# Performance work log

Hardware: AMD Instinct MI355X
Metric: run time of the kernel (lower is better)

## Reference

```python
import math
import jax, jax.numpy as jnp
import numpy as np

B, QC, KC, RES, SRC = 4, 512, 256, 64, 128
T = RES * RES


def setup_inputs():
    key = jax.random.key(0)
    ks = jax.random.split(key, 8)
    return {
        "key_feat": jax.random.normal(ks[0], (B, KC, SRC, SRC), jnp.float32),
        "query": jax.random.normal(ks[1], (B, QC, RES, RES), jnp.float32),
        "Weight_Mat": jax.random.uniform(ks[2], (B, T, T), dtype=jnp.float32),
        "key_proj_w": jax.random.normal(ks[3], (QC, KC), jnp.float32) * 0.02,
        "norm_w": jnp.ones((QC,), jnp.float32),
        "norm_b": jnp.zeros((QC,), jnp.float32),
        "qkv_w": jax.random.normal(ks[4], (3 * QC, 2 * QC), jnp.float32) * 0.02,
        "qkv_b": jax.random.normal(ks[5], (3 * QC,), jnp.float32) * 0.02,
        "proj_w": jax.random.normal(ks[6], (QC, QC), jnp.float32) * 0.02,
        "proj_b": jnp.zeros((QC,), jnp.float32),
    }


def group_norm(x, w, b, groups=32, eps=1e-5):
    # x: (b, C, L) -- GroupNorm over channel groups and spatial dim
    bs, C, L = x.shape
    xg = x.reshape(bs, groups, C // groups, L)
    mu = xg.mean(axis=(2, 3), keepdims=True)
    var = xg.var(axis=(2, 3), keepdims=True)
    xn = ((xg - mu) * jax.lax.rsqrt(var + eps)).reshape(bs, C, L)
    return xn * w[None, :, None] + b[None, :, None]


def reference(key_feat, query, Weight_Mat, key_proj_w, norm_w, norm_b, qkv_w, qkv_b, proj_w, proj_b):
    b, qc, H, W = query.shape
    f = key_feat.shape[2] // H  # exact integer downsample factor (2)
    # F.interpolate bilinear (align_corners=False) at exact 1/f rate == f x f average pooling
    kds = key_feat.reshape(b, key_feat.shape[1], H, f, W, f).mean(axis=(3, 5))
    # Weight_Mat interpolate has scale==1 in source (no-op), elided.
    k = jnp.einsum('oc,bchw->bohw', key_proj_w, kds).reshape(b, qc, H * W)
    q = query.reshape(b, qc, H * W)
    q = group_norm(q, norm_w, norm_b)
    k = group_norm(k, norm_w, norm_b)
    # qkv: 1x1 conv1d on concat(q, k) -> (b, 3*qc, T)
    qkv = jnp.einsum('oc,bct->bot', qkv_w, jnp.concatenate([q, k], axis=1)) + qkv_b[None, :, None]
    qq, kk, vv = jnp.split(qkv, 3, axis=1)  # each (b, qc, T); num_heads=1 so ch=qc
    scale = qc ** -0.25  # 1/sqrt(sqrt(ch))
    logits = Weight_Mat * jnp.einsum('bct,bcs->bts', qq * scale, kk * scale)
    attn = jax.nn.softmax(logits, axis=-1)
    a = jnp.einsum('bts,bcs->bct', attn, vv)
    h = jnp.einsum('oc,bct->bot', proj_w, a) + proj_b[None, :, None]
    # residual uses the NORMALIZED query, as in the source
    return (q + h).reshape(b, qc, H, W)
```

## Files before the change

### kernel.cpp

```cpp
#include <hip/hip_runtime.h>
#include <hip/hip_bf16.h>
#include <stdint.h>

#define NB 4
#define CQ 512
#define CK 256
#define TT 4096
#define SCALE_QK 0.21022410381342863f

using bf16x8 = __attribute__((ext_vector_type(8))) short;
using f32x4  = __attribute__((ext_vector_type(4))) float;
using u32x4  = __attribute__((ext_vector_type(4))) unsigned int;
typedef unsigned short u16;

__device__ __forceinline__ u16 f2bf(float f) {
    union { float f; unsigned u; } v; v.f = f;
    return (u16)((v.u + 0x7fffu + ((v.u >> 16) & 1u)) >> 16);
}
__device__ __forceinline__ float bf2f(u16 h) {
    union { float f; unsigned u; } v; v.u = ((unsigned)h) << 16;
    return v.f;
}
__device__ __forceinline__ bf16x8 pack8(f32x4 a, f32x4 b) {
    bf16x8 r;
    r[0] = (short)f2bf(a[0]); r[1] = (short)f2bf(a[1]);
    r[2] = (short)f2bf(a[2]); r[3] = (short)f2bf(a[3]);
    r[4] = (short)f2bf(b[0]); r[5] = (short)f2bf(b[1]);
    r[6] = (short)f2bf(b[2]); r[7] = (short)f2bf(b[3]);
    return r;
}
__device__ __forceinline__ void gload_lds16(const void* g, void* l) {
    __builtin_amdgcn_global_load_lds(
        (const __attribute__((address_space(1))) unsigned int*)g,
        (__attribute__((address_space(3))) unsigned int*)l, 16, 0, 0);
}

__global__ __launch_bounds__(256) void wconv_kernel(const float* __restrict__ src,
        u16* __restrict__ dst, int n, int scale_until) {
    int i = (blockIdx.x * 256 + threadIdx.x) * 8;
    if (i >= n) return;
    f32x4 a = *(const f32x4*)(src + i);
    f32x4 c = *(const f32x4*)(src + i + 4);
    if (i < scale_until) {
        a *= SCALE_QK;
        c *= SCALE_QK;
    }
    *(bf16x8*)(dst + i) = pack8(a, c);
}

__global__ __launch_bounds__(256) void pool_tr_kernel(const float* __restrict__ kf,
                                                      u16* __restrict__ kdsT) {
    int h = blockIdx.x, b = blockIdx.y;
    __shared__ u16 tile[64][264];
    for (int idx = threadIdx.x; idx < 64 * 256; idx += 256) {
        int w = idx & 63, c = idx >> 6;
        const float* base = kf + (((size_t)b * CK + c) * 128 + 2 * h) * 128 + 2 * w;
        float2 r0 = *(const float2*)base;
        float2 r1 = *(const float2*)(base + 128);
        tile[w][c] = f2bf(0.25f * (r0.x + r0.y + r1.x + r1.y));
    }
    __syncthreads();
    for (int idx = threadIdx.x; idx < 64 * 32; idx += 256) {
        int w = idx >> 5, cg = (idx & 31) << 3;
        *(u32x4*)(kdsT + ((size_t)b * TT + h * 64 + w) * CK + cg) = *(const u32x4*)&tile[w][cg];
    }
}

template <int ISBF>
__global__ __launch_bounds__(256) void gn_stats_kernel(const void* __restrict__ xv,
        const float* __restrict__ gw, const float* __restrict__ gb,
        float* __restrict__ sc, float* __restrict__ sh) {
    int g = blockIdx.x, b = blockIdx.y;
    size_t base = ((size_t)b * CQ + g * 16) * TT;
    float s = 0.f, q = 0.f;
    for (int i = threadIdx.x * 4; i < 16 * TT; i += 256 * 4) {
        float v0, v1, v2, v3;
        if constexpr (ISBF) {
            const u16* x = (const u16*)xv;
            uint2 u = *(const uint2*)(x + base + i);
            v0 = bf2f((u16)(u.x & 0xffff)); v1 = bf2f((u16)(u.x >> 16));
            v2 = bf2f((u16)(u.y & 0xffff)); v3 = bf2f((u16)(u.y >> 16));
        } else {
            const float* x = (const float*)xv;
            f32x4 v = *(const f32x4*)(x + base + i);
            v0 = v[0]; v1 = v[1]; v2 = v[2]; v3 = v[3];
        }
        s += v0 + v1 + v2 + v3;
        q += v0 * v0 + v1 * v1 + v2 * v2 + v3 * v3;
    }
#pragma unroll
    for (int d = 1; d < 64; d <<= 1) { s += __shfl_xor(s, d, 64); q += __shfl_xor(q, d, 64); }
    __shared__ float shs[4], shq[4];
    int wid = threadIdx.x >> 6;
    if ((threadIdx.x & 63) == 0) { shs[wid] = s; shq[wid] = q; }
    __syncthreads();
    if (threadIdx.x < 16) {
        float S = shs[0] + shs[1] + shs[2] + shs[3];
        float Q = shq[0] + shq[1] + shq[2] + shq[3];
        const float inv = 1.f / (16.f * TT);
        float mean = S * inv, var = Q * inv - mean * mean;
        float rstd = rsqrtf(var + 1e-5f);
        int c = g * 16 + threadIdx.x;
        float w = gw[c] * rstd;
        sc[b * CQ + c] = w;
        sh[b * CQ + c] = gb[c] - mean * w;
    }
}

template <int ISBF>
__global__ __launch_bounds__(256) void affine_tr_kernel(const void* __restrict__ xv,
        const float* __restrict__ sc, const float* __restrict__ sh, u16* __restrict__ out) {
    int t0 = blockIdx.x * 64, c0 = blockIdx.y * 64, b = blockIdx.z;
    __shared__ u16 tile[64][72];
    for (int idx = threadIdx.x; idx < 64 * 64; idx += 256) {
        int tl = idx & 63, cl = idx >> 6;
        int c = c0 + cl;
        float v;
        if constexpr (ISBF) v = bf2f(((const u16*)xv)[((size_t)b * CQ + c) * TT + t0 + tl]);
        else                v = ((const float*)xv)[((size_t)b * CQ + c) * TT + t0 + tl];
        tile[tl][cl] = f2bf(v * sc[b * CQ + c] + sh[b * CQ + c]);
    }
    __syncthreads();
    for (int idx = threadIdx.x; idx < 64 * 8; idx += 256) {
        int tl = idx >> 3, cg = (idx & 7) << 3;
        *(u32x4*)(out + ((size_t)b * TT + t0 + tl) * CQ + c0 + cg) = *(const u32x4*)&tile[tl][cg];
    }
}

template <int EPI, int CONCAT, int SWAP>
__global__ __launch_bounds__(256) void gemm_st_kernel(
        const u16* __restrict__ Wb, const u16* __restrict__ X1, const u16* __restrict__ X2,
        int Ktot, const float* __restrict__ bias,
        u16* __restrict__ outb, u16* __restrict__ outb2, float* __restrict__ outf,
        const float* __restrict__ query, const float* __restrict__ qsc,
        const float* __restrict__ qsh) {
    int b = blockIdx.z;
    int o0 = blockIdx.x * 128, t0 = blockIdx.y * 128;
    int wid = threadIdx.x >> 6, lane = threadIdx.x & 63;
    int lr = lane & 15, lg = lane >> 4;
    int osub = (wid >> 1) * 64, tsub = (wid & 1) * 64;

    __shared__ u16 Wl[2][128][64];
    __shared__ u16 Xl[2][128][64];

    const int Kx = CONCAT ? 512 : Ktot;
    int srow = lane >> 3;
    int sxw = ((lane & 7) ^ srow) << 4;
    int xr = (lr & 7) << 4;

    f32x4 acc[4][4];
#pragma unroll
    for (int i = 0; i < 4; i++)
#pragma unroll
        for (int j = 0; j < 4; j++) acc[i][j] = f32x4{0.f, 0.f, 0.f, 0.f};

    int nk = Ktot >> 6;

#define STAGE_TILE(KC, BUF)                                                          \
    do {                                                                             \
        int c0_ = (KC) << 6;                                                         \
        const u16* xs_;                                                              \
        if (CONCAT && c0_ >= 512) xs_ = X2 + ((size_t)b * TT) * 512 + (c0_ - 512);   \
        else if (CONCAT)          xs_ = X1 + ((size_t)b * TT) * 512 + c0_;           \
        else                      xs_ = X1 + ((size_t)b * TT) * (size_t)Ktot + c0_;  \
        const char* xb_ = (const char*)(xs_ + (size_t)(t0 + wid * 32) * Kx) + sxw;   \
        const char* wb_ = (const char*)(Wb + (size_t)(o0 + wid * 32) * Ktot + c0_) + sxw; \
        _Pragma("unroll")                                                            \
        for (int i_ = 0; i_ < 4; i_++) {                                             \
            gload_lds16(xb_ + (size_t)(i_ * 8 + srow) * (Kx * 2),                    \
                        &Xl[BUF][wid * 32 + i_ * 8][0]);                             \
            gload_lds16(wb_ + (size_t)(i_ * 8 + srow) * (Ktot * 2),                  \
                        &Wl[BUF][wid * 32 + i_ * 8][0]);                             \
        }                                                                            \
    } while (0)

    STAGE_TILE(0, 0);
    __syncthreads();
    int cur = 0;
    for (int kc = 0; kc < nk; kc++) {
        if (kc + 1 < nk) STAGE_TILE(kc + 1, cur ^ 1);
#pragma unroll
        for (int kk = 0; kk < 2; kk++) {
            int boff = (kk * 64 + lg * 16) ^ xr;
            bf16x8 am[4], bn[4];
#pragma unroll
            for (int mi = 0; mi < 4; mi++) {
                if (SWAP) am[mi] = *(const bf16x8*)((const char*)&Xl[cur][tsub + mi * 16 + lr][0] + boff);
                else      am[mi] = *(const bf16x8*)((const char*)&Wl[cur][osub + mi * 16 + lr][0] + boff);
            }
#pragma unroll
            for (int ni = 0; ni < 4; ni++) {
                if (SWAP) bn[ni] = *(const bf16x8*)((const char*)&Wl[cur][osub + ni * 16 + lr][0] + boff);
                else      bn[ni] = *(const bf16x8*)((const char*)&Xl[cur][tsub + ni * 16 + lr][0] + boff);
            }
#pragma unroll
            for (int mi = 0; mi < 4; mi++)
#pragma unroll
                for (int ni = 0; ni < 4; ni++)
                    acc[mi][ni] = __builtin_amdgcn_mfma_f32_16x16x32_bf16(am[mi], bn[ni], acc[mi][ni], 0, 0, 0);
        }
        __syncthreads();
        cur ^= 1;
    }
#undef STAGE_TILE

    if (SWAP) {
#pragma unroll
        for (int mi = 0; mi < 4; mi++)
#pragma unroll
            for (int ni = 0; ni < 4; ni++)
#pragma unroll
                for (int reg = 0; reg < 4; reg++) {
                    int t = t0 + tsub + mi * 16 + 4 * lg + reg;
                    int o = o0 + osub + ni * 16 + lr;
                    float v = acc[mi][ni][reg] + bias[o] * SCALE_QK;
                    if (o < 512) outb[((size_t)b * TT + t) * 512 + o] = f2bf(v);
                    else         outb2[((size_t)b * TT + t) * 512 + (o - 512)] = f2bf(v);
                }
    } else {
#pragma unroll
        for (int mi = 0; mi < 4; mi++)
#pragma unroll
            for (int reg = 0; reg < 4; reg++) {
                int o = o0 + osub + mi * 16 + 4 * lg + reg;
                float bv = (EPI >= 1) ? bias[o] : 0.f;
#pragma unroll
                for (int ni = 0; ni < 4; ni++) {
                    int t = t0 + tsub + ni * 16 + lr;
                    size_t oidx = ((size_t)b * CQ + o) * TT + t;
                    float v = acc[mi][ni][reg] + bv;
                    if (EPI == 2) {
                        outf[oidx] = v + query[oidx] * qsc[b * CQ + o] + qsh[b * CQ + o];
                    } else {
                        outb[oidx] = f2bf(v);
                    }
                }
            }
    }
}

__global__ __launch_bounds__(512, 2) void flash_kernel(
        const u16* __restrict__ qqT, const u16* __restrict__ kkT,
        const u16* __restrict__ vv, const float* __restrict__ WM,
        u16* __restrict__ aT) {
    int b = blockIdx.y;
    int T0 = blockIdx.x * 64;
    int wid = threadIdx.x >> 6, lane = threadIdx.x & 63;
    int lr = lane & 15, lg = lane >> 4;
    int tb = wid >> 1, sb = wid & 1;

    __shared__ u16 K_lds[64][512];
    __shared__ u16 V_lds[512][64];
    __shared__ u16 p_lds[64][64];
    __shared__ float ex_max[64][2];
    __shared__ float ex_sum[64][2];

    bf16x8 qf[16];
    {
        const u16* qrow = qqT + ((size_t)b * TT + T0 + 16 * tb + lr) * CQ + lg * 8;
#pragma unroll
        for (int kc = 0; kc < 16; kc++) qf[kc] = *(const bf16x8*)(qrow + kc * 32);
    }
    f32x4 acc[16];
#pragma unroll
    for (int i = 0; i < 16; i++) acc[i] = f32x4{0.f, 0.f, 0.f, 0.f};
    float m[4], l[4];
#pragma unroll
    for (int r = 0; r < 4; r++) { m[r] = -1e30f; l[r] = 0.f; }

    const float* wmrow = WM + ((size_t)b * TT + T0 + 16 * tb + 4 * lg) * TT + 32 * sb + lr;
    const char* kbase = (const char*)(kkT + ((size_t)b * TT) * CQ);
    int myt = 16 * tb + 4 * lg;

    for (int s0 = 0; s0 < TT; s0 += 64) {
        __syncthreads();
#pragma unroll
        for (int i = 0; i < 8; i++) {
            int s = wid * 8 + i;
            gload_lds16(kbase + ((size_t)(s0 + s)) * 1024 + ((lane ^ (s & 7)) << 4),
                        &K_lds[s][0]);
        }
#pragma unroll
        for (int g2 = 0; g2 < 8; g2++) {
            int c0 = (wid * 8 + g2) * 8;
            int c = c0 + (lane >> 3);
            gload_lds16((const char*)(vv + ((size_t)b * CQ + c) * TT + s0) +
                            ((((lane & 7) ^ (c & 7))) << 4),
                        &V_lds[c0][0]);
        }
        float wmv[2][4];
#pragma unroll
        for (int fs = 0; fs < 2; fs++)
#pragma unroll
            for (int reg = 0; reg < 4; reg++)
                wmv[fs][reg] = wmrow[(size_t)reg * TT + s0 + fs * 16];
        __syncthreads();

        f32x4 sacc[2];
        sacc[0] = f32x4{0.f, 0.f, 0.f, 0.f};
        sacc[1] = f32x4{0.f, 0.f, 0.f, 0.f};
#pragma unroll
        for (int kc = 0; kc < 16; kc++) {
#pragma unroll
            for (int fs = 0; fs < 2; fs++) {
                const char* kp = (const char*)&K_lds[32 * sb + fs * 16 + lr][0];
                bf16x8 kfr = *(const bf16x8*)(kp + ((((kc << 2) | lg) ^ (lr & 7)) << 4));
                sacc[fs] = __builtin_amdgcn_mfma_f32_16x16x32_bf16(qf[kc], kfr, sacc[fs], 0, 0, 0);
            }
        }
        float lgt[2][4], pmax[4];
#pragma unroll
        for (int r = 0; r < 4; r++) pmax[r] = -3e38f;
#pragma unroll
        for (int fs = 0; fs < 2; fs++)
#pragma unroll
            for (int reg = 0; reg < 4; reg++) {
                float v = sacc[fs][reg] * wmv[fs][reg];
                lgt[fs][reg] = v;
                pmax[reg] = fmaxf(pmax[reg], v);
            }
#pragma unroll
        for (int d = 1; d < 16; d <<= 1)
#pragma unroll
            for (int reg = 0; reg < 4; reg++)
                pmax[reg] = fmaxf(pmax[reg], __shfl_xor(pmax[reg], d, 64));
        if (lr == 0) {
#pragma unroll
            for (int reg = 0; reg < 4; reg++) ex_max[myt + reg][sb] = pmax[reg];
        }
        __syncthreads();
        float fac[4], rsum[4];
#pragma unroll
        for (int reg = 0; reg < 4; reg++) {
            int t = myt + reg;
            float mn = fmaxf(m[reg], fmaxf(ex_max[t][0], ex_max[t][1]));
            fac[reg] = __expf(m[reg] - mn);
            m[reg] = mn;
            rsum[reg] = 0.f;
        }
#pragma unroll
        for (int fs = 0; fs < 2; fs++)
#pragma unroll
            for (int reg = 0; reg < 4; reg++) {
                float p = __expf(lgt[fs][reg] - m[reg]);
                rsum[reg] += p;
                int t = myt + reg;
                int s = 32 * sb + fs * 16 + lr;
                *(u16*)((char*)p_lds + t * 128 + ((((s >> 3) ^ (t & 7))) << 4) + ((s & 7) << 1)) = f2bf(p);
            }
#pragma unroll
        for (int d = 1; d < 16; d <<= 1)
#pragma unroll
            for (int reg = 0; reg < 4; reg++)
                rsum[reg] += __shfl_xor(rsum[reg], d, 64);
        if (lr == 0) {
#pragma unroll
            for (int reg = 0; reg < 4; reg++) ex_sum[myt + reg][sb] = rsum[reg];
        }
        __syncthreads();
#pragma unroll
        for (int reg = 0; reg < 4; reg++) {
            int t = myt + reg;
            l[reg] = l[reg] * fac[reg] + ex_sum[t][0] + ex_sum[t][1];
        }
#pragma unroll
        for (int nt = 0; nt < 16; nt++)
#pragma unroll
            for (int reg = 0; reg < 4; reg++) acc[nt][reg] *= fac[reg];
#pragma unroll
        for (int ks = 0; ks < 2; ks++) {
            int prow = 16 * tb + lr;
            bf16x8 pa = *(const bf16x8*)((const char*)p_lds + prow * 128 +
                                         ((((ks << 2) | lg) ^ (lr & 7)) << 4));
#pragma unroll
            for (int nt = 0; nt < 16; nt++) {
                int vr = 256 * sb + nt * 16 + lr;
                bf16x8 vf = *(const bf16x8*)((const char*)&V_lds[vr][0] +
                                             ((((ks << 2) | lg) ^ (lr & 7)) << 4));
                acc[nt] = __builtin_amdgcn_mfma_f32_16x16x32_bf16(pa, vf, acc[nt], 0, 0, 0);
            }
        }
    }
    float inv[4];
#pragma unroll
    for (int reg = 0; reg < 4; reg++) inv[reg] = 1.f / l[reg];
#pragma unroll
    for (int nt = 0; nt < 16; nt++)
#pragma unroll
        for (int reg = 0; reg < 4; reg++) {
            int t = T0 + myt + reg;
            int c = 256 * sb + nt * 16 + lr;
            aT[((size_t)b * TT + t) * CQ + c] = f2bf(acc[nt][reg] * inv[reg]);
        }
}

extern "C" void kernel_launch(void* const* d_in, const int* in_sizes, int n_in,
                              void* d_out, int out_size, void* d_ws, size_t ws_size,
                              hipStream_t stream) {
    const float* key_feat = (const float*)d_in[0];
    const float* query    = (const float*)d_in[1];
    const float* WM       = (const float*)d_in[2];
    const float* kpw      = (const float*)d_in[3];
    const float* norm_w   = (const float*)d_in[4];
    const float* norm_b   = (const float*)d_in[5];
    const float* qkv_w    = (const float*)d_in[6];
    const float* qkv_b    = (const float*)d_in[7];
    const float* proj_w   = (const float*)d_in[8];
    const float* proj_b   = (const float*)d_in[9];
    float* out = (float*)d_out;
    char* ws = (char*)d_ws;

    u16* kdsT = (u16*)(ws);
    u16* kraw = (u16*)(ws + 8388608);
    u16* qnT  = (u16*)(ws + 25165824);
    u16* knT  = (u16*)(ws + 41943040);
    u16* qqT  = (u16*)(ws + 58720256);
    u16* kkT  = (u16*)(ws + 75497472);
    u16* vvp  = (u16*)(ws + 92274688);
    u16* aT   = (u16*)(ws);
    u16* wqkv = (u16*)(ws + 16777216);
    u16* wproj= (u16*)(ws + 19922944);
    float* qsc = (float*)(ws + 109051904);
    float* qsh = qsc + NB * CQ;
    float* ksc = qsh + NB * CQ;
    float* ksh = ksc + NB * CQ;
    u16* wkp  = (u16*)(ws + 109084672);

    wconv_kernel<<<64, 256, 0, stream>>>(kpw, wkp, 512 * 256, 0);
    pool_tr_kernel<<<dim3(64, NB), 256, 0, stream>>>(key_feat, kdsT);
    gemm_st_kernel<0, 0, 0><<<dim3(4, 32, NB), 256, 0, stream>>>(
        wkp, kdsT, nullptr, CK, nullptr, kraw, nullptr, nullptr, nullptr, nullptr, nullptr);
    gn_stats_kernel<0><<<dim3(32, NB), 256, 0, stream>>>(query, norm_w, norm_b, qsc, qsh);
    gn_stats_kernel<1><<<dim3(32, NB), 256, 0, stream>>>(kraw, norm_w, norm_b, ksc, ksh);
    affine_tr_kernel<0><<<dim3(64, 8, NB), 256, 0, stream>>>(query, qsc, qsh, qnT);
    affine_tr_kernel<1><<<dim3(64, 8, NB), 256, 0, stream>>>(kraw, ksc, ksh, knT);
    wconv_kernel<<<768, 256, 0, stream>>>(qkv_w, wqkv, 1536 * 1024, 1024 * 1024);
    wconv_kernel<<<128, 256, 0, stream>>>(proj_w, wproj, 512 * 512, 0);
    gemm_st_kernel<1, 1, 1><<<dim3(8, 32, NB), 256, 0, stream>>>(
        wqkv, qnT, knT, 1024, qkv_b, qqT, kkT, nullptr, nullptr, nullptr, nullptr);
    gemm_st_kernel<1, 1, 0><<<dim3(4, 32, NB), 256, 0, stream>>>(
        wqkv + (size_t)1024 * 1024, qnT, knT, 1024, qkv_b + 1024, vvp, nullptr, nullptr,
        nullptr, nullptr, nullptr);
    flash_kernel<<<dim3(64, NB), 512, 0, stream>>>(qqT, kkT, vvp, WM, aT);
    gemm_st_kernel<2, 0, 0><<<dim3(4, 32, NB), 256, 0, stream>>>(
        wproj, aT, nullptr, CQ, proj_b, nullptr, nullptr, out, query, qsc, qsh);
}
```

Baseline: 543.9 us.

## Double-buffer K/V tiles with 32-wide steps and skip redundant rescales

The flash attention loop now uses 32-key tiles held in two LDS buffers. The next tile's K, V and Weight_Mat loads are issued before computing on the current tile, and custom barriers wait only on partial vmcnt, so global loads overlap with MFMA work. The accumulator rescale is skipped when no row max changed in the wave, and the LDS swizzles are adjusted for the narrower tiles. The cost is twice as many iterations and barriers per tile of work, and a dependence on hand-written waitcnt counts being correct.

```diff
diff --git a/kernel.cpp b/kernel.cpp
--- a/kernel.cpp
+++ b/kernel.cpp
@@ -33,6 +33,12 @@
     __builtin_amdgcn_global_load_lds(
         (const __attribute__((address_space(1))) unsigned int*)g,
         (__attribute__((address_space(3))) unsigned int*)l, 16, 0, 0);
+}
+__device__ __forceinline__ void bar_lg() {
+    asm volatile("s_waitcnt lgkmcnt(0)\n\ts_barrier" ::: "memory");
+}
+__device__ __forceinline__ void bar_vm12() {
+    asm volatile("s_waitcnt vmcnt(12) lgkmcnt(0)\n\ts_barrier" ::: "memory");
 }
 
 __global__ __launch_bounds__(256) void wconv_kernel(const float* __restrict__ src,
@@ -249,9 +255,9 @@
     int lr = lane & 15, lg = lane >> 4;
     int tb = wid >> 1, sb = wid & 1;
 
-    __shared__ u16 K_lds[64][512];
-    __shared__ u16 V_lds[512][64];
-    __shared__ u16 p_lds[64][64];
+    __shared__ u16 Kl[2][32][512];
+    __shared__ u16 Vl[2][512][32];
+    __shared__ u16 p_lds[64][32];
     __shared__ float ex_max[64][2];
     __shared__ float ex_sum[64][2];
 
@@ -268,57 +274,65 @@
 #pragma unroll
     for (int r = 0; r < 4; r++) { m[r] = -1e30f; l[r] = 0.f; }
 
-    const float* wmrow = WM + ((size_t)b * TT + T0 + 16 * tb + 4 * lg) * TT + 32 * sb + lr;
-    const char* kbase = (const char*)(kkT + ((size_t)b * TT) * CQ);
+    const char* kbase = (const char*)(kkT + (size_t)b * TT * CQ);
+    const char* vbase = (const char*)(vv + (size_t)b * CQ * TT);
+    const float* wmbase = WM + ((size_t)b * TT + T0 + 16 * tb + 4 * lg) * TT + 16 * sb + lr;
     int myt = 16 * tb + 4 * lg;
 
-    for (int s0 = 0; s0 < TT; s0 += 64) {
-        __syncthreads();
-#pragma unroll
-        for (int i = 0; i < 8; i++) {
-            int s = wid * 8 + i;
-            gload_lds16(kbase + ((size_t)(s0 + s)) * 1024 + ((lane ^ (s & 7)) << 4),
-                        &K_lds[s][0]);
-        }
-#pragma unroll
-        for (int g2 = 0; g2 < 8; g2++) {
-            int c0 = (wid * 8 + g2) * 8;
-            int c = c0 + (lane >> 3);
-            gload_lds16((const char*)(vv + ((size_t)b * CQ + c) * TT + s0) +
-                            ((((lane & 7) ^ (c & 7))) << 4),
-                        &V_lds[c0][0]);
-        }
-        float wmv[2][4];
-#pragma unroll
-        for (int fs = 0; fs < 2; fs++)
-#pragma unroll
-            for (int reg = 0; reg < 4; reg++)
-                wmv[fs][reg] = wmrow[(size_t)reg * TT + s0 + fs * 16];
-        __syncthreads();
-
-        f32x4 sacc[2];
-        sacc[0] = f32x4{0.f, 0.f, 0.f, 0.f};
-        sacc[1] = f32x4{0.f, 0.f, 0.f, 0.f};
-#pragma unroll
-        for (int kc = 0; kc < 16; kc++) {
-#pragma unroll
-            for (int fs = 0; fs < 2; fs++) {
-                const char* kp = (const char*)&K_lds[32 * sb + fs * 16 + lr][0];
+    auto STAGE = [&](int s0, int buf) {
+#pragma unroll
+        for (int i = 0; i < 4; i++) {
+            int s = 4 * wid + i;
+            gload_lds16(kbase + (size_t)(s0 + s) * 1024 + ((lane ^ (s & 7)) << 4),
+                        &Kl[buf][s][0]);
+        }
+#pragma unroll
+        for (int g = 0; g < 4; g++) {
+            int c0 = 64 * wid + 16 * g;
+            int c = c0 + (lane >> 2);
+            gload_lds16(vbase + (size_t)c * (TT * 2) + (size_t)s0 * 2 +
+                            ((((lane & 3) ^ ((c >> 1) & 3))) << 4),
+                        &Vl[buf][c0][0]);
+        }
+    };
+    float wmn[4];
+    auto WMLOAD = [&](int s0) {
+#pragma unroll
+        for (int r = 0; r < 4; r++) wmn[r] = wmbase[(size_t)r * TT + s0];
+    };
+
+    STAGE(0, 0);
+    WMLOAD(0);
+
+    int cur = 0;
+#pragma unroll 1
+    for (int it = 0; it < TT / 32; it++) {
+        int s0 = it * 32;
+        bar_lg();
+        float wmv[4];
+#pragma unroll
+        for (int r = 0; r < 4; r++) wmv[r] = wmn[r];
+        int sn = (s0 + 32 < TT) ? s0 + 32 : 0;
+        STAGE(sn, cur ^ 1);
+        WMLOAD(sn);
+        bar_vm12();
+
+        f32x4 sacc = f32x4{0.f, 0.f, 0.f, 0.f};
+        {
+            const char* kp = (const char*)&Kl[cur][16 * sb + lr][0];
+#pragma unroll
+            for (int kc = 0; kc < 16; kc++) {
                 bf16x8 kfr = *(const bf16x8*)(kp + ((((kc << 2) | lg) ^ (lr & 7)) << 4));
-                sacc[fs] = __builtin_amdgcn_mfma_f32_16x16x32_bf16(qf[kc], kfr, sacc[fs], 0, 0, 0);
+                sacc = __builtin_amdgcn_mfma_f32_16x16x32_bf16(qf[kc], kfr, sacc, 0, 0, 0);
             }
         }
-        float lgt[2][4], pmax[4];
-#pragma unroll
-        for (int r = 0; r < 4; r++) pmax[r] = -3e38f;
-#pragma unroll
-        for (int fs = 0; fs < 2; fs++)
-#pragma unroll
-            for (int reg = 0; reg < 4; reg++) {
-                float v = sacc[fs][reg] * wmv[fs][reg];
-                lgt[fs][reg] = v;
-                pmax[reg] = fmaxf(pmax[reg], v);
-            }
+        float lgt[4], pmax[4];
+#pragma unroll
+        for (int reg = 0; reg < 4; reg++) {
+            float v = sacc[reg] * wmv[reg];
+            lgt[reg] = v;
+            pmax[reg] = v;
+        }
 #pragma unroll
         for (int d = 1; d < 16; d <<= 1)
 #pragma unroll
@@ -328,26 +342,27 @@
 #pragma unroll
             for (int reg = 0; reg < 4; reg++) ex_max[myt + reg][sb] = pmax[reg];
         }
-        __syncthreads();
+        bar_lg();
         float fac[4], rsum[4];
+        bool need = false;
 #pragma unroll
         for (int reg = 0; reg < 4; reg++) {
             int t = myt + reg;
-            float mn = fmaxf(m[reg], fmaxf(ex_max[t][0], ex_max[t][1]));
-            fac[reg] = __expf(m[reg] - mn);
-            m[reg] = mn;
-            rsum[reg] = 0.f;
-        }
-#pragma unroll
-        for (int fs = 0; fs < 2; fs++)
-#pragma unroll
-            for (int reg = 0; reg < 4; reg++) {
-                float p = __expf(lgt[fs][reg] - m[reg]);
-                rsum[reg] += p;
-                int t = myt + reg;
-                int s = 32 * sb + fs * 16 + lr;
-                *(u16*)((char*)p_lds + t * 128 + ((((s >> 3) ^ (t & 7))) << 4) + ((s & 7) << 1)) = f2bf(p);
-            }
+            float mo = m[reg];
+            float mn2 = fmaxf(mo, fmaxf(ex_max[t][0], ex_max[t][1]));
+            fac[reg] = __expf(mo - mn2);
+            need = need || (mn2 > mo);
+            m[reg] = mn2;
+        }
+#pragma unroll
+        for (int reg = 0; reg < 4; reg++) {
+            float p = __expf(lgt[reg] - m[reg]);
+            rsum[reg] = p;
+            int t = myt + reg;
+            int s = 16 * sb + lr;
+            int sw = ((t >> 2) & 3) << 3;
+            *(u16*)((char*)p_lds + t * 64 + ((s ^ sw) << 1)) = f2bf(p);
+        }
 #pragma unroll
         for (int d = 1; d < 16; d <<= 1)
 #pragma unroll
@@ -357,29 +372,31 @@
 #pragma unroll
             for (int reg = 0; reg < 4; reg++) ex_sum[myt + reg][sb] = rsum[reg];
         }
-        __syncthreads();
+        bar_lg();
 #pragma unroll
         for (int reg = 0; reg < 4; reg++) {
             int t = myt + reg;
             l[reg] = l[reg] * fac[reg] + ex_sum[t][0] + ex_sum[t][1];
         }
-#pragma unroll
-        for (int nt = 0; nt < 16; nt++)
-#pragma unroll
-            for (int reg = 0; reg < 4; reg++) acc[nt][reg] *= fac[reg];
-#pragma unroll
-        for (int ks = 0; ks < 2; ks++) {
-            int prow = 16 * tb + lr;
-            bf16x8 pa = *(const bf16x8*)((const char*)p_lds + prow * 128 +
-                                         ((((ks << 2) | lg) ^ (lr & 7)) << 4));
+        if (__any(need)) {
+#pragma unroll
+            for (int nt = 0; nt < 16; nt++)
+#pragma unroll
+                for (int reg = 0; reg < 4; reg++) acc[nt][reg] *= fac[reg];
+        }
+        {
+            int t = 16 * tb + lr;
+            bf16x8 pa = *(const bf16x8*)((const char*)p_lds + t * 64 +
+                                         ((lg ^ ((lr >> 2) & 3)) << 4));
+            const char* vb = (const char*)&Vl[cur][0][0];
 #pragma unroll
             for (int nt = 0; nt < 16; nt++) {
                 int vr = 256 * sb + nt * 16 + lr;
-                bf16x8 vf = *(const bf16x8*)((const char*)&V_lds[vr][0] +
-                                             ((((ks << 2) | lg) ^ (lr & 7)) << 4));
+                bf16x8 vf = *(const bf16x8*)(vb + vr * 64 + ((lg ^ ((lr >> 1) & 3)) << 4));
                 acc[nt] = __builtin_amdgcn_mfma_f32_16x16x32_bf16(pa, vf, acc[nt], 0, 0, 0);
             }
         }
+        cur ^= 1;
     }
     float inv[4];
 #pragma unroll
```

Result: slower. 657.4 us (+20.9%).

## Use lazy softmax rescaling with stale max and retile PV as 32x128 per wave

Applied to the files above, without the earlier changes.

Probabilities are now computed against the previous row max read from shared memory. This merges the max and sum reductions and removes one block barrier per key tile. The accumulator is rescaled only when the new max exceeds the stored one by more than 8, and the running max is published back to shared memory for the next tile. The PV product is re-tiled so each wave covers 32 rows by 128 channels, which reuses each V fragment across two MFMAs and halves V LDS reads. The trade-off is exposure to exp overflow if logits run far above the initial zero max, plus a little extra bookkeeping.

```diff
diff --git a/kernel.cpp b/kernel.cpp
--- a/kernel.cpp
+++ b/kernel.cpp
@@ -248,12 +248,16 @@
     int wid = threadIdx.x >> 6, lane = threadIdx.x & 63;
     int lr = lane & 15, lg = lane >> 4;
     int tb = wid >> 1, sb = wid & 1;
+    int tb2 = wid >> 2, sbq = wid & 3;
 
     __shared__ u16 K_lds[64][512];
     __shared__ u16 V_lds[512][64];
     __shared__ u16 p_lds[64][64];
     __shared__ float ex_max[64][2];
     __shared__ float ex_sum[64][2];
+    __shared__ float m_lds[64];
+
+    if (threadIdx.x < 64) m_lds[threadIdx.x] = 0.f;
 
     bf16x8 qf[16];
     {
@@ -261,15 +265,19 @@
 #pragma unroll
         for (int kc = 0; kc < 16; kc++) qf[kc] = *(const bf16x8*)(qrow + kc * 32);
     }
-    f32x4 acc[16];
-#pragma unroll
-    for (int i = 0; i < 16; i++) acc[i] = f32x4{0.f, 0.f, 0.f, 0.f};
-    float m[4], l[4];
-#pragma unroll
-    for (int r = 0; r < 4; r++) { m[r] = -1e30f; l[r] = 0.f; }
+    f32x4 acc[2][8];
+#pragma unroll
+    for (int i = 0; i < 2; i++)
+#pragma unroll
+        for (int j = 0; j < 8; j++) acc[i][j] = f32x4{0.f, 0.f, 0.f, 0.f};
+    float m[2][4], l[2][4];
+#pragma unroll
+    for (int i = 0; i < 2; i++)
+#pragma unroll
+        for (int r = 0; r < 4; r++) { m[i][r] = 0.f; l[i][r] = 0.f; }
 
     const float* wmrow = WM + ((size_t)b * TT + T0 + 16 * tb + 4 * lg) * TT + 32 * sb + lr;
-    const char* kbase = (const char*)(kkT + ((size_t)b * TT) * CQ);
+    const char* kbase = (const char*)(kkT + (size_t)b * TT * CQ);
     int myt = 16 * tb + 4 * lg;
 
     for (int s0 = 0; s0 < TT; s0 += 64) {
@@ -277,7 +285,7 @@
 #pragma unroll
         for (int i = 0; i < 8; i++) {
             int s = wid * 8 + i;
-            gload_lds16(kbase + ((size_t)(s0 + s)) * 1024 + ((lane ^ (s & 7)) << 4),
+            gload_lds16(kbase + (size_t)(s0 + s) * 1024 + ((lane ^ (s & 7)) << 4),
                         &K_lds[s][0]);
         }
 #pragma unroll
@@ -294,6 +302,9 @@
 #pragma unroll
             for (int reg = 0; reg < 4; reg++)
                 wmv[fs][reg] = wmrow[(size_t)reg * TT + s0 + fs * 16];
+        float mq[4];
+#pragma unroll
+        for (int reg = 0; reg < 4; reg++) mq[reg] = m_lds[myt + reg];
         __syncthreads();
 
         f32x4 sacc[2];
@@ -308,42 +319,17 @@
                 sacc[fs] = __builtin_amdgcn_mfma_f32_16x16x32_bf16(qf[kc], kfr, sacc[fs], 0, 0, 0);
             }
         }
-        float lgt[2][4], pmax[4];
-#pragma unroll
-        for (int r = 0; r < 4; r++) pmax[r] = -3e38f;
+        float pmax[4], psum[4];
+#pragma unroll
+        for (int r = 0; r < 4; r++) { pmax[r] = -3e38f; psum[r] = 0.f; }
 #pragma unroll
         for (int fs = 0; fs < 2; fs++)
 #pragma unroll
             for (int reg = 0; reg < 4; reg++) {
                 float v = sacc[fs][reg] * wmv[fs][reg];
-                lgt[fs][reg] = v;
                 pmax[reg] = fmaxf(pmax[reg], v);
-            }
-#pragma unroll
-        for (int d = 1; d < 16; d <<= 1)
-#pragma unroll
-            for (int reg = 0; reg < 4; reg++)
-                pmax[reg] = fmaxf(pmax[reg], __shfl_xor(pmax[reg], d, 64));
-        if (lr == 0) {
-#pragma unroll
-            for (int reg = 0; reg < 4; reg++) ex_max[myt + reg][sb] = pmax[reg];
-        }
-        __syncthreads();
-        float fac[4], rsum[4];
-#pragma unroll
-        for (int reg = 0; reg < 4; reg++) {
-            int t = myt + reg;
-            float mn = fmaxf(m[reg], fmaxf(ex_max[t][0], ex_max[t][1]));
-            fac[reg] = __expf(m[reg] - mn);
-            m[reg] = mn;
-            rsum[reg] = 0.f;
-        }
-#pragma unroll
-        for (int fs = 0; fs < 2; fs++)
-#pragma unroll
-            for (int reg = 0; reg < 4; reg++) {
-                float p = __expf(lgt[fs][reg] - m[reg]);
-                rsum[reg] += p;
+                float p = __expf(v - mq[reg]);
+                psum[reg] += p;
                 int t = myt + reg;
                 int s = 32 * sb + fs * 16 + lr;
                 *(u16*)((char*)p_lds + t * 128 + ((((s >> 3) ^ (t & 7))) << 4) + ((s & 7) << 1)) = f2bf(p);
@@ -351,47 +337,88 @@
 #pragma unroll
         for (int d = 1; d < 16; d <<= 1)
 #pragma unroll
-            for (int reg = 0; reg < 4; reg++)
-                rsum[reg] += __shfl_xor(rsum[reg], d, 64);
+            for (int reg = 0; reg < 4; reg++) {
+                pmax[reg] = fmaxf(pmax[reg], __shfl_xor(pmax[reg], d, 64));
+                psum[reg] += __shfl_xor(psum[reg], d, 64);
+            }
         if (lr == 0) {
 #pragma unroll
-            for (int reg = 0; reg < 4; reg++) ex_sum[myt + reg][sb] = rsum[reg];
+            for (int reg = 0; reg < 4; reg++) {
+                ex_max[myt + reg][sb] = pmax[reg];
+                ex_sum[myt + reg][sb] = psum[reg];
+            }
         }
         __syncthreads();
-#pragma unroll
-        for (int reg = 0; reg < 4; reg++) {
-            int t = myt + reg;
-            l[reg] = l[reg] * fac[reg] + ex_sum[t][0] + ex_sum[t][1];
-        }
-#pragma unroll
-        for (int nt = 0; nt < 16; nt++)
-#pragma unroll
-            for (int reg = 0; reg < 4; reg++) acc[nt][reg] *= fac[reg];
+
 #pragma unroll
         for (int ks = 0; ks < 2; ks++) {
-            int prow = 16 * tb + lr;
-            bf16x8 pa = *(const bf16x8*)((const char*)p_lds + prow * 128 +
-                                         ((((ks << 2) | lg) ^ (lr & 7)) << 4));
-#pragma unroll
-            for (int nt = 0; nt < 16; nt++) {
-                int vr = 256 * sb + nt * 16 + lr;
+            bf16x8 pa[2];
+#pragma unroll
+            for (int mi = 0; mi < 2; mi++) {
+                int prow = 32 * tb2 + mi * 16 + lr;
+                pa[mi] = *(const bf16x8*)((const char*)p_lds + prow * 128 +
+                                          ((((ks << 2) | lg) ^ (lr & 7)) << 4));
+            }
+#pragma unroll
+            for (int nc = 0; nc < 8; nc++) {
+                int vr = 128 * sbq + nc * 16 + lr;
                 bf16x8 vf = *(const bf16x8*)((const char*)&V_lds[vr][0] +
                                              ((((ks << 2) | lg) ^ (lr & 7)) << 4));
-                acc[nt] = __builtin_amdgcn_mfma_f32_16x16x32_bf16(pa, vf, acc[nt], 0, 0, 0);
-            }
-        }
-    }
-    float inv[4];
-#pragma unroll
-    for (int reg = 0; reg < 4; reg++) inv[reg] = 1.f / l[reg];
-#pragma unroll
-    for (int nt = 0; nt < 16; nt++)
-#pragma unroll
-        for (int reg = 0; reg < 4; reg++) {
-            int t = T0 + myt + reg;
-            int c = 256 * sb + nt * 16 + lr;
-            aT[((size_t)b * TT + t) * CQ + c] = f2bf(acc[nt][reg] * inv[reg]);
-        }
+#pragma unroll
+                for (int mi = 0; mi < 2; mi++)
+                    acc[mi][nc] = __builtin_amdgcn_mfma_f32_16x16x32_bf16(pa[mi], vf, acc[mi][nc], 0, 0, 0);
+            }
+        }
+        bool needany = false;
+        float fac[2][4];
+#pragma unroll
+        for (int mi = 0; mi < 2; mi++)
+#pragma unroll
+            for (int reg = 0; reg < 4; reg++) {
+                int t = 32 * tb2 + mi * 16 + 4 * lg + reg;
+                float pm = fmaxf(ex_max[t][0], ex_max[t][1]);
+                l[mi][reg] += ex_sum[t][0] + ex_sum[t][1];
+                if (pm > m[mi][reg] + 8.f) {
+                    fac[mi][reg] = __expf(m[mi][reg] - pm);
+                    m[mi][reg] = pm;
+                    needany = true;
+                } else {
+                    fac[mi][reg] = 1.f;
+                }
+            }
+        if (__any(needany)) {
+#pragma unroll
+            for (int mi = 0; mi < 2; mi++)
+#pragma unroll
+                for (int reg = 0; reg < 4; reg++) {
+                    l[mi][reg] *= fac[mi][reg];
+#pragma unroll
+                    for (int nc = 0; nc < 8; nc++) acc[mi][nc][reg] *= fac[mi][reg];
+                }
+            if (lr == 0) {
+#pragma unroll
+                for (int mi = 0; mi < 2; mi++)
+#pragma unroll
+                    for (int reg = 0; reg < 4; reg++)
+                        m_lds[32 * tb2 + mi * 16 + 4 * lg + reg] = m[mi][reg];
+            }
+        }
+    }
+    float inv[2][4];
+#pragma unroll
+    for (int mi = 0; mi < 2; mi++)
+#pragma unroll
+        for (int reg = 0; reg < 4; reg++) inv[mi][reg] = 1.f / l[mi][reg];
+#pragma unroll
+    for (int mi = 0; mi < 2; mi++)
+#pragma unroll
+        for (int nc = 0; nc < 8; nc++)
+#pragma unroll
+            for (int reg = 0; reg < 4; reg++) {
+                int t = T0 + 32 * tb2 + mi * 16 + 4 * lg + reg;
+                int c = 128 * sbq + nc * 16 + lr;
+                aT[((size_t)b * TT + t) * CQ + c] = f2bf(acc[mi][nc][reg] * inv[mi][reg]);
+            }
 }
 
 extern "C" void kernel_launch(void* const* d_in, const int* in_sizes, int n_in,
```

New measurement: 551.8 us. No clear change (+1.4%).
